# Optimization experiments

Hardware: AMD Instinct MI355X
Metric: run time of the kernel (lower is better)

## Reference

```python
import jax, jax.numpy as jnp
import numpy as np
from jax import lax

B, S, D, K = 4, 4096, 2048, 4


def setup_inputs() -> dict:
    key = jax.random.key(0)
    k1, k2, k3 = jax.random.split(key, 3)
    x = jax.random.normal(k1, (B, S, D), dtype=jnp.float32)
    # torch Conv1d(dim, dim, K, groups=dim) weight shape: [dim, 1, K]
    weight = jax.random.normal(k2, (D, 1, K), dtype=jnp.float32) * (1.0 / np.sqrt(K))
    bias = jax.random.normal(k3, (D,), dtype=jnp.float32) * 0.02
    return {"x": x, "weight": weight, "bias": bias}


def reference(x, weight, bias):
    # x: [B, S, D] -> [B, D, S] (NCH); causal left pad K-1; depthwise conv.
    xc = jnp.transpose(x, (0, 2, 1))  # [B, D, S]
    out = lax.conv_general_dilated(
        xc, weight,
        window_strides=(1,),
        padding=[(K - 1, 0)],  # causal: left pad only
        dimension_numbers=("NCH", "OIH", "NCH"),
        feature_group_count=D,
    )  # [B, D, S]
    out = out + bias[None, :, None]
    return jnp.transpose(out, (0, 2, 1))  # [B, S, D]
```

## Files before the change

kernel.cpp:

```cpp
#include <hip/hip_runtime.h>
#include <hip/hip_bf16.h>


typedef float vfloat4 __attribute__((ext_vector_type(4)));

namespace {
constexpr int B = 4;
constexpr int S = 4096;
constexpr int D = 2048;
constexpr int D4 = D / 4;
constexpr int R = 16;
constexpr int BLOCK = 256;
}

__global__ __launch_bounds__(BLOCK) void causal_dwconv1d_k4(
    const vfloat4* __restrict__ x,
    const vfloat4* __restrict__ w4,
    const vfloat4* __restrict__ bias4,
    vfloat4* __restrict__ out)
{
    const int d4 = blockIdx.x * BLOCK + threadIdx.x;
    const int s0 = blockIdx.y * R;
    const int b  = blockIdx.z;

    const vfloat4* xb = x   + (size_t)b * S * D4 + d4;
    vfloat4*       ob = out + (size_t)b * S * D4 + d4;

    const vfloat4 zero = (vfloat4)(0.f);

    vfloat4 xr[R + 3];
    if (s0 >= 3) {
#pragma unroll
        for (int i = 0; i < R + 3; ++i)
            xr[i] = xb[(size_t)(s0 - 3 + i) * D4];
    } else {
#pragma unroll
        for (int i = 0; i < R + 3; ++i) {
            const int s = s0 - 3 + i;
            xr[i] = (s >= 0) ? xb[(size_t)s * D4] : zero;
        }
    }

    const vfloat4 wa = w4[d4 * 4 + 0];
    const vfloat4 wb = w4[d4 * 4 + 1];
    const vfloat4 wc = w4[d4 * 4 + 2];
    const vfloat4 wd = w4[d4 * 4 + 3];
    const vfloat4 bv = bias4[d4];

#pragma unroll
    for (int r = 0; r < R; ++r) {
        const vfloat4 xm3 = xr[r + 0];
        const vfloat4 xm2 = xr[r + 1];
        const vfloat4 xm1 = xr[r + 2];
        const vfloat4 xc  = xr[r + 3];
        vfloat4 o;
        o.x = bv.x + wa.x * xm3.x + wa.y * xm2.x + wa.z * xm1.x + wa.w * xc.x;
        o.y = bv.y + wb.x * xm3.y + wb.y * xm2.y + wb.z * xm1.y + wb.w * xc.y;
        o.z = bv.z + wc.x * xm3.z + wc.y * xm2.z + wc.z * xm1.z + wc.w * xc.z;
        o.w = bv.w + wd.x * xm3.w + wd.y * xm2.w + wd.z * xm1.w + wd.w * xc.w;
        __builtin_nontemporal_store(o, &ob[(size_t)(s0 + r) * D4]);
    }
}

extern "C" void kernel_launch(void* const* d_in, const int* in_sizes, int n_in,
                              void* d_out, int out_size, void* d_ws, size_t ws_size,
                              hipStream_t stream) {
    const vfloat4* x     = (const vfloat4*)d_in[0];
    const vfloat4* w4    = (const vfloat4*)d_in[1];
    const vfloat4* bias4 = (const vfloat4*)d_in[2];
    vfloat4* out         = (vfloat4*)d_out;

    dim3 grid(D4 / BLOCK, S / R, B);
    dim3 block(BLOCK);
    causal_dwconv1d_k4<<<grid, block, 0, stream>>>(x, w4, bias4, out);
}
```

Before: 238.8 us.

## Stream sequence strip with double-buffered chunk loads and sliding register window

Each thread now handles a 32-row strip instead of 16. It loads rows in chunks of 4, prefetching the next chunk while computing the current one, and keeps a three-row sliding window in registers, which cuts the halo re-read overhead and register pressure. Nontemporal stores are replaced with ordinary stores. The trade-off is half as many blocks, less memory-level parallelism per thread than loading all 19 rows up front, and possible cache pollution from the normal stores.

```diff
diff --git a/kernel.cpp b/kernel.cpp
--- a/kernel.cpp
+++ b/kernel.cpp
@@ -9,7 +9,9 @@
 constexpr int S = 4096;
 constexpr int D = 2048;
 constexpr int D4 = D / 4;
-constexpr int R = 16;
+constexpr int CH = 4;
+constexpr int NCH = 8;
+constexpr int STRIP = CH * NCH;
 constexpr int BLOCK = 256;
 }
 
@@ -20,7 +22,7 @@
     vfloat4* __restrict__ out)
 {
     const int d4 = blockIdx.x * BLOCK + threadIdx.x;
-    const int s0 = blockIdx.y * R;
+    const int s0 = blockIdx.y * STRIP;
     const int b  = blockIdx.z;
 
     const vfloat4* xb = x   + (size_t)b * S * D4 + d4;
@@ -28,38 +30,54 @@
 
     const vfloat4 zero = (vfloat4)(0.f);
 
-    vfloat4 xr[R + 3];
-    if (s0 >= 3) {
-#pragma unroll
-        for (int i = 0; i < R + 3; ++i)
-            xr[i] = xb[(size_t)(s0 - 3 + i) * D4];
-    } else {
-#pragma unroll
-        for (int i = 0; i < R + 3; ++i) {
-            const int s = s0 - 3 + i;
-            xr[i] = (s >= 0) ? xb[(size_t)s * D4] : zero;
-        }
-    }
-
     const vfloat4 wa = w4[d4 * 4 + 0];
     const vfloat4 wb = w4[d4 * 4 + 1];
     const vfloat4 wc = w4[d4 * 4 + 2];
     const vfloat4 wd = w4[d4 * 4 + 3];
     const vfloat4 bv = bias4[d4];
 
-#pragma unroll
-    for (int r = 0; r < R; ++r) {
-        const vfloat4 xm3 = xr[r + 0];
-        const vfloat4 xm2 = xr[r + 1];
-        const vfloat4 xm1 = xr[r + 2];
-        const vfloat4 xc  = xr[r + 3];
+    vfloat4 xm3, xm2, xm1;
+    if (s0 >= 3) {
+        xm3 = xb[(size_t)(s0 - 3) * D4];
+        xm2 = xb[(size_t)(s0 - 2) * D4];
+        xm1 = xb[(size_t)(s0 - 1) * D4];
+    } else {
+        xm3 = zero; xm2 = zero; xm1 = zero;
+    }
+
+    auto row = [&](const vfloat4 xc, int s) {
         vfloat4 o;
         o.x = bv.x + wa.x * xm3.x + wa.y * xm2.x + wa.z * xm1.x + wa.w * xc.x;
         o.y = bv.y + wb.x * xm3.y + wb.y * xm2.y + wb.z * xm1.y + wb.w * xc.y;
         o.z = bv.z + wc.x * xm3.z + wc.y * xm2.z + wc.z * xm1.z + wc.w * xc.z;
         o.w = bv.w + wd.x * xm3.w + wd.y * xm2.w + wd.z * xm1.w + wd.w * xc.w;
-        __builtin_nontemporal_store(o, &ob[(size_t)(s0 + r) * D4]);
+        ob[(size_t)s * D4] = o;
+        xm3 = xm2; xm2 = xm1; xm1 = xc;
+    };
+
+    vfloat4 c0 = xb[(size_t)(s0 + 0) * D4];
+    vfloat4 c1 = xb[(size_t)(s0 + 1) * D4];
+    vfloat4 c2 = xb[(size_t)(s0 + 2) * D4];
+    vfloat4 c3 = xb[(size_t)(s0 + 3) * D4];
+
+    for (int c = 0; c < NCH - 1; ++c) {
+        const int sn = s0 + (c + 1) * CH;
+        const vfloat4 n0 = xb[(size_t)(sn + 0) * D4];
+        const vfloat4 n1 = xb[(size_t)(sn + 1) * D4];
+        const vfloat4 n2 = xb[(size_t)(sn + 2) * D4];
+        const vfloat4 n3 = xb[(size_t)(sn + 3) * D4];
+        const int sc = s0 + c * CH;
+        row(c0, sc + 0);
+        row(c1, sc + 1);
+        row(c2, sc + 2);
+        row(c3, sc + 3);
+        c0 = n0; c1 = n1; c2 = n2; c3 = n3;
     }
+    const int sc = s0 + (NCH - 1) * CH;
+    row(c0, sc + 0);
+    row(c1, sc + 1);
+    row(c2, sc + 2);
+    row(c3, sc + 3);
 }
 
 extern "C" void kernel_launch(void* const* d_in, const int* in_sizes, int n_in,
@@ -70,7 +88,7 @@
     const vfloat4* bias4 = (const vfloat4*)d_in[2];
     vfloat4* out         = (vfloat4*)d_out;
 
-    dim3 grid(D4 / BLOCK, S / R, B);
+    dim3 grid(D4 / BLOCK, S / STRIP, B);
     dim3 block(BLOCK);
     causal_dwconv1d_k4<<<grid, block, 0, stream>>>(x, w4, bias4, out);
 }
```

Measured after the change: 239.2 us. Within noise of the previous version (+0.2%).

## Stage input tile into LDS via direct global-to-LDS loads

Applied to the files above, without the earlier changes.

Replaces per-thread register loads of the input window with wave-cooperative global_load_lds transfers into a shared tile, then reads rows from LDS with a rolling register window. Nontemporal stores become plain stores, and the launch bounds now request two blocks per CU. The intent is to cut VGPR pressure and issue more memory traffic in parallel. The cost is about 76KB of LDS per block, a full barrier, and direct-to-LDS loads of 16 bytes per lane, which may not be supported on this hardware. The shared-tile writes for zero-padded rows rely on the same barrier.

```diff
diff --git a/kernel.cpp b/kernel.cpp
--- a/kernel.cpp
+++ b/kernel.cpp
@@ -10,55 +10,67 @@
 constexpr int D = 2048;
 constexpr int D4 = D / 4;
 constexpr int R = 16;
+constexpr int HALO = 3;
+constexpr int ROWS = R + HALO;
+constexpr int COLS = 256;
 constexpr int BLOCK = 256;
 }
 
-__global__ __launch_bounds__(BLOCK) void causal_dwconv1d_k4(
+__global__ __launch_bounds__(BLOCK, 2) void causal_dwconv1d_k4(
     const vfloat4* __restrict__ x,
     const vfloat4* __restrict__ w4,
     const vfloat4* __restrict__ bias4,
     vfloat4* __restrict__ out)
 {
-    const int d4 = blockIdx.x * BLOCK + threadIdx.x;
-    const int s0 = blockIdx.y * R;
-    const int b  = blockIdx.z;
+    __shared__ vfloat4 tile[ROWS][COLS];
 
-    const vfloat4* xb = x   + (size_t)b * S * D4 + d4;
-    vfloat4*       ob = out + (size_t)b * S * D4 + d4;
+    const int tid  = threadIdx.x;
+    const int wave = tid >> 6;
+    const int lane = tid & 63;
+    const int col0 = blockIdx.x * COLS;
+    const int s0   = blockIdx.y * R;
+    const int b    = blockIdx.z;
 
-    const vfloat4 zero = (vfloat4)(0.f);
+    const vfloat4* xb = x   + (size_t)b * S * D4 + col0;
+    vfloat4*       ob = out + (size_t)b * S * D4 + col0;
 
-    vfloat4 xr[R + 3];
-    if (s0 >= 3) {
-#pragma unroll
-        for (int i = 0; i < R + 3; ++i)
-            xr[i] = xb[(size_t)(s0 - 3 + i) * D4];
-    } else {
-#pragma unroll
-        for (int i = 0; i < R + 3; ++i) {
-            const int s = s0 - 3 + i;
-            xr[i] = (s >= 0) ? xb[(size_t)s * D4] : zero;
+    const int c = tid;
+    const vfloat4 wa = w4[(col0 + c) * 4 + 0];
+    const vfloat4 wb = w4[(col0 + c) * 4 + 1];
+    const vfloat4 wc = w4[(col0 + c) * 4 + 2];
+    const vfloat4 wd = w4[(col0 + c) * 4 + 3];
+    const vfloat4 bv = bias4[col0 + c];
+
+    for (int i = wave; i < ROWS * 4; i += 4) {
+        const int row = i >> 2;
+        const int ch  = (i & 3) * 64;
+        const int s   = s0 - HALO + row;
+        if (s >= 0) {
+            const vfloat4* src = xb + (size_t)s * D4 + ch + lane;
+            __builtin_amdgcn_global_load_lds(
+                (const __attribute__((address_space(1))) void*)src,
+                (__attribute__((address_space(3))) void*)&tile[row][ch],
+                16, 0, 0);
+        } else {
+            tile[row][ch + lane] = (vfloat4)(0.f);
         }
     }
 
-    const vfloat4 wa = w4[d4 * 4 + 0];
-    const vfloat4 wb = w4[d4 * 4 + 1];
-    const vfloat4 wc = w4[d4 * 4 + 2];
-    const vfloat4 wd = w4[d4 * 4 + 3];
-    const vfloat4 bv = bias4[d4];
+    __syncthreads();
 
+    vfloat4 xm3 = tile[0][c];
+    vfloat4 xm2 = tile[1][c];
+    vfloat4 xm1 = tile[2][c];
 #pragma unroll
     for (int r = 0; r < R; ++r) {
-        const vfloat4 xm3 = xr[r + 0];
-        const vfloat4 xm2 = xr[r + 1];
-        const vfloat4 xm1 = xr[r + 2];
-        const vfloat4 xc  = xr[r + 3];
+        const vfloat4 xc = tile[r + HALO][c];
         vfloat4 o;
         o.x = bv.x + wa.x * xm3.x + wa.y * xm2.x + wa.z * xm1.x + wa.w * xc.x;
         o.y = bv.y + wb.x * xm3.y + wb.y * xm2.y + wb.z * xm1.y + wb.w * xc.y;
         o.z = bv.z + wc.x * xm3.z + wc.y * xm2.z + wc.z * xm1.z + wc.w * xc.z;
         o.w = bv.w + wd.x * xm3.w + wd.y * xm2.w + wd.z * xm1.w + wd.w * xc.w;
-        __builtin_nontemporal_store(o, &ob[(size_t)(s0 + r) * D4]);
+        ob[(size_t)(s0 + r) * D4 + c] = o;
+        xm3 = xm2; xm2 = xm1; xm1 = xc;
     }
 }
 
@@ -70,7 +82,7 @@
     const vfloat4* bias4 = (const vfloat4*)d_in[2];
     vfloat4* out         = (vfloat4*)d_out;
 
-    dim3 grid(D4 / BLOCK, S / R, B);
+    dim3 grid(D4 / COLS, S / R, B);
     dim3 block(BLOCK);
     causal_dwconv1d_k4<<<grid, block, 0, stream>>>(x, w4, bias4, out);
 }
```

New measurement: 239.5 us. About the same (+0.3%).
